# Performance work log

Hardware: AMD Instinct MI355X
Metric: run time of the kernel (lower is better)

The kernel has to match this reference:

```python
import jax, jax.numpy as jnp
import numpy as np

N = 40000   # num_words
H = 384     # hidden_dim
D = 20000   # num_docs
E = 800000  # word-word edges
NNZ = 800000  # doc-word tfidf entries
ALPHA = 0.65
EPS = 1e-5


def layernorm(x, g, b):
    m = jnp.mean(x, axis=-1, keepdims=True)
    v = jnp.mean((x - m) ** 2, axis=-1, keepdims=True)
    return (x - m) * jax.lax.rsqrt(v + EPS) * g + b


def gelu(x):
    return jax.nn.gelu(x, approximate=False)  # torch F.gelu default (erf)


def spmm(rows, cols, vals, M, n_out):
    # COO sparse [n_out, n_in] @ dense [n_in, H]
    return jax.ops.segment_sum(vals[:, None] * M[cols], rows, num_segments=n_out)


def setup_inputs() -> dict:
    key = jax.random.key(0)
    ks = jax.random.split(key, 24)
    s = 1.0 / np.sqrt(H)
    inp = {
        "A_rows": jax.random.randint(ks[0], (E,), 0, N, dtype=jnp.int32),
        "A_cols": jax.random.randint(ks[1], (E,), 0, N, dtype=jnp.int32),
        "A_vals": jax.random.uniform(ks[2], (E,), jnp.float32),
        "X_rows": jax.random.randint(ks[3], (NNZ,), 0, D, dtype=jnp.int32),
        "X_cols": jax.random.randint(ks[4], (NNZ,), 0, N, dtype=jnp.int32),
        "X_vals": jax.random.uniform(ks[5], (NNZ,), jnp.float32),
        "num_docs": D,
        "emb": jax.random.normal(ks[6], (N, H), jnp.float32) * s,
        "W1": jax.random.normal(ks[7], (H, H), jnp.float32) * s,
        "W2": jax.random.normal(ks[8], (H, H), jnp.float32) * s,
        "W3": jax.random.normal(ks[9], (H, H), jnp.float32) * s,
        "g1": jnp.ones((H,), jnp.float32), "b1": jnp.zeros((H,), jnp.float32),
        "g2": jnp.ones((H,), jnp.float32), "b2": jnp.zeros((H,), jnp.float32),
        "g3": jnp.ones((H,), jnp.float32), "b3": jnp.zeros((H,), jnp.float32),
        "mlp_W1": jax.random.normal(ks[10], (H, H), jnp.float32) * s,
        "mlp_b1": jnp.zeros((H,), jnp.float32),
        "mlp_g": jnp.ones((H,), jnp.float32), "mlp_bn": jnp.zeros((H,), jnp.float32),
        "mlp_W2": jax.random.normal(ks[11], (H, H // 2), jnp.float32) * s,
        "mlp_b2": jnp.zeros((H // 2,), jnp.float32),
        "cls_W": jax.random.normal(ks[12], (H // 2, 2), jnp.float32) * s,
        "cls_b": jnp.zeros((2,), jnp.float32),
        "gate_W1": jax.random.normal(ks[13], (2 * H, H), jnp.float32) * s,
        "gate_b1": jnp.zeros((H,), jnp.float32),
        "gate_W2": jax.random.normal(ks[14], (H, H), jnp.float32) * s,
        "gate_b2": jnp.zeros((H,), jnp.float32),
    }
    return inp


def reference(A_rows, A_cols, A_vals, X_rows, X_cols, X_vals, num_docs, emb,
              W1, W2, W3, g1, b1, g2, b2, g3, b3,
              mlp_W1, mlp_b1, mlp_g, mlp_bn, mlp_W2, mlp_b2,
              cls_W, cls_b, gate_W1, gate_b1, gate_W2, gate_b2):
    n = emb.shape[0]
    # --- 3 residual GCN blocks over word graph (eval mode: dropout off) ---
    h = spmm(A_rows, A_cols, A_vals, emb, n)
    h = gelu(layernorm(h @ W1, g1, b1))
    h = spmm(A_rows, A_cols, A_vals, h, n)
    h = gelu(layernorm(h @ W2, g2, b2))
    h = spmm(A_rows, A_cols, A_vals, h, n)
    h = gelu(layernorm(h @ W3, g3, b3))
    word_H = (1.0 - ALPHA) * emb + ALPHA * h
    # --- doc aggregation via TF-IDF SpMM ---
    doc_H = spmm(X_rows, X_cols, X_vals, word_H, num_docs)
    doc_H0 = spmm(X_rows, X_cols, X_vals, emb, num_docs)
    gate_in = jnp.concatenate([doc_H, doc_H0], axis=1)
    gate = jax.nn.sigmoid(gelu(gate_in @ gate_W1 + gate_b1) @ gate_W2 + gate_b2)
    doc = gate * doc_H + (1.0 - gate) * doc_H0
    # --- MLP head ---
    doc = layernorm(gelu(doc @ mlp_W1 + mlp_b1), mlp_g, mlp_bn)
    doc = gelu(doc @ mlp_W2 + mlp_b2)
    logits = doc @ cls_W + cls_b
    return logits
```

## Files before the change

### kernel.cpp

```cpp
#include <hip/hip_runtime.h>
#include <hip/hip_fp16.h>

#define HD 384
#define HHD 192
#define TPR 96
#define RPB 4
#define ECHUNK 128

using bf16x8 = __attribute__((ext_vector_type(8))) short;
using f32x4  = __attribute__((ext_vector_type(4))) float;

__device__ __forceinline__ float gelu_f(float x) {
    return 0.5f * x * (1.0f + erff(x * 0.70710678118654752f));
}

__device__ __forceinline__ float sigmoid_f(float x) {
    return 1.0f / (1.0f + expf(-x));
}

__device__ __forceinline__ void ld_h4(const __half2* p, float2& lo, float2& hi) {
    uint2 raw = *reinterpret_cast<const uint2*>(p);
    lo = __half22float2(*reinterpret_cast<const __half2*>(&raw.x));
    hi = __half22float2(*reinterpret_cast<const __half2*>(&raw.y));
}

__global__ __launch_bounds__(256) void hist_rows(
        const int* __restrict__ rows, int* __restrict__ cnt, int nnz) {
    int e = blockIdx.x * blockDim.x + threadIdx.x;
    if (e < nnz) atomicAdd(&cnt[rows[e]], 1);
}

__global__ __launch_bounds__(256) void scan_local(
        const int* __restrict__ cnt, int* __restrict__ rp,
        int* __restrict__ bsum, int n) {
    __shared__ int wsum[4];
    int i = blockIdx.x * 256 + threadIdx.x;
    int lane = threadIdx.x & 63, wv = threadIdx.x >> 6;
    int v = (i < n) ? cnt[i] : 0;
    int s = v;
    #pragma unroll
    for (int o = 1; o < 64; o <<= 1) {
        int t = __shfl_up(s, o);
        if (lane >= o) s += t;
    }
    if (lane == 63) wsum[wv] = s;
    __syncthreads();
    int woff = 0;
    for (int w = 0; w < wv; ++w) woff += wsum[w];
    if (i < n) rp[i] = woff + s - v;
    if (threadIdx.x == 255) bsum[blockIdx.x] = woff + s;
}

__global__ __launch_bounds__(256) void scan_bsums(
        const int* __restrict__ bsum, int* __restrict__ boff,
        int nb, int* __restrict__ total_out) {
    __shared__ int tmp[256];
    int tid = threadIdx.x;
    int v = (tid < nb) ? bsum[tid] : 0;
    tmp[tid] = v;
    __syncthreads();
    for (int o = 1; o < 256; o <<= 1) {
        int t = (tid >= o) ? tmp[tid - o] : 0;
        __syncthreads();
        tmp[tid] += t;
        __syncthreads();
    }
    if (tid < nb) boff[tid] = tmp[tid] - v;
    if (tid == nb - 1) *total_out = tmp[tid];
}

__global__ __launch_bounds__(256) void scan_add(
        int* __restrict__ rp, const int* __restrict__ boff, int n) {
    int i = blockIdx.x * 256 + threadIdx.x;
    if (i < n) rp[i] += boff[i >> 8];
}

__global__ __launch_bounds__(256) void csr_scatter(
        const int* __restrict__ rows, const int* __restrict__ cols,
        const float* __restrict__ vals, const int* __restrict__ rp,
        int* __restrict__ fill, int* __restrict__ cp,
        float* __restrict__ vp, int nnz) {
    int e = blockIdx.x * blockDim.x + threadIdx.x;
    if (e >= nnz) return;
    int r = rows[e];
    int pos = rp[r] + atomicAdd(&fill[r], 1);
    cp[pos] = cols[e];
    vp[pos] = vals[e];
}

__global__ __launch_bounds__(256) void cvt_fp16(
        const float* __restrict__ in, __half2* __restrict__ out, int n2) {
    int i = blockIdx.x * blockDim.x + threadIdx.x;
    if (i >= n2) return;
    float2 v = reinterpret_cast<const float2*>(in)[i];
    out[i] = __floats2half2_rn(v.x, v.y);
}

__global__ __launch_bounds__(384) void spmm_h2(
        const int* __restrict__ rp, const int* __restrict__ cp,
        const float* __restrict__ vp, const __half2* __restrict__ in,
        __half2* __restrict__ out, int nrows) {
    __shared__ int   lc[RPB][ECHUNK];
    __shared__ float lv[RPB][ECHUNK];
    __shared__ int maxlen_s;
    const int rr = threadIdx.x / TPR;
    const int t  = threadIdx.x % TPR;
    const int r  = blockIdx.x * RPB + rr;
    int s = 0, len = 0;
    if (r < nrows) { s = rp[r]; len = rp[r + 1] - s; }
    if (threadIdx.x == 0) maxlen_s = 0;
    __syncthreads();
    if (t == 0) atomicMax(&maxlen_s, len);
    __syncthreads();
    const int nch = (maxlen_s + ECHUNK - 1) / ECHUNK;
    float a0 = 0.f, a1 = 0.f, a2 = 0.f, a3 = 0.f;
    for (int ch = 0; ch < nch; ++ch) {
        const int base = ch * ECHUNK;
        const int tile = min(ECHUNK, len - base);
        for (int i = t; i < tile; i += TPR) {
            lc[rr][i] = cp[s + base + i];
            lv[rr][i] = vp[s + base + i];
        }
        __syncthreads();
        int p = 0;
        for (; p + 4 <= tile; p += 4) {
            int   c0 = lc[rr][p],     c1 = lc[rr][p + 1];
            int   c2 = lc[rr][p + 2], c3 = lc[rr][p + 3];
            float v0 = lv[rr][p],     v1 = lv[rr][p + 1];
            float v2 = lv[rr][p + 2], v3 = lv[rr][p + 3];
            float2 x0l, x0h, x1l, x1h, x2l, x2h, x3l, x3h;
            ld_h4(in + (size_t)c0 * HHD + 2 * t, x0l, x0h);
            ld_h4(in + (size_t)c1 * HHD + 2 * t, x1l, x1h);
            ld_h4(in + (size_t)c2 * HHD + 2 * t, x2l, x2h);
            ld_h4(in + (size_t)c3 * HHD + 2 * t, x3l, x3h);
            a0 = fmaf(v0, x0l.x, a0); a1 = fmaf(v0, x0l.y, a1);
            a2 = fmaf(v0, x0h.x, a2); a3 = fmaf(v0, x0h.y, a3);
            a0 = fmaf(v1, x1l.x, a0); a1 = fmaf(v1, x1l.y, a1);
            a2 = fmaf(v1, x1h.x, a2); a3 = fmaf(v1, x1h.y, a3);
            a0 = fmaf(v2, x2l.x, a0); a1 = fmaf(v2, x2l.y, a1);
            a2 = fmaf(v2, x2h.x, a2); a3 = fmaf(v2, x2h.y, a3);
            a0 = fmaf(v3, x3l.x, a0); a1 = fmaf(v3, x3l.y, a1);
            a2 = fmaf(v3, x3h.x, a2); a3 = fmaf(v3, x3h.y, a3);
        }
        for (; p < tile; ++p) {
            int c = lc[rr][p];
            float v = lv[rr][p];
            float2 xl, xh;
            ld_h4(in + (size_t)c * HHD + 2 * t, xl, xh);
            a0 = fmaf(v, xl.x, a0); a1 = fmaf(v, xl.y, a1);
            a2 = fmaf(v, xh.x, a2); a3 = fmaf(v, xh.y, a3);
        }
        __syncthreads();
    }
    if (r < nrows) {
        __half2 o0 = __floats2half2_rn(a0, a1);
        __half2 o1 = __floats2half2_rn(a2, a3);
        uint2 packed;
        packed.x = *reinterpret_cast<unsigned*>(&o0);
        packed.y = *reinterpret_cast<unsigned*>(&o1);
        *reinterpret_cast<uint2*>(out + (size_t)r * HHD + 2 * t) = packed;
    }
}

__global__ __launch_bounds__(384) void spmm_doc2(
        const int* __restrict__ rp, const int* __restrict__ cp,
        const float* __restrict__ vp,
        const __half2* __restrict__ inH, const __half2* __restrict__ inE,
        float* __restrict__ docH, float* __restrict__ docH0, int nrows) {
    __shared__ int   lc[RPB][ECHUNK];
    __shared__ float lv[RPB][ECHUNK];
    __shared__ int maxlen_s;
    const int rr = threadIdx.x / TPR;
    const int t  = threadIdx.x % TPR;
    const int r  = blockIdx.x * RPB + rr;
    int s = 0, len = 0;
    if (r < nrows) { s = rp[r]; len = rp[r + 1] - s; }
    if (threadIdx.x == 0) maxlen_s = 0;
    __syncthreads();
    if (t == 0) atomicMax(&maxlen_s, len);
    __syncthreads();
    const int nch = (maxlen_s + ECHUNK - 1) / ECHUNK;
    float h0 = 0.f, h1 = 0.f, h2 = 0.f, h3 = 0.f;
    float e0 = 0.f, e1 = 0.f, e2 = 0.f, e3 = 0.f;
    for (int ch = 0; ch < nch; ++ch) {
        const int base = ch * ECHUNK;
        const int tile = min(ECHUNK, len - base);
        for (int i = t; i < tile; i += TPR) {
            lc[rr][i] = cp[s + base + i];
            lv[rr][i] = vp[s + base + i];
        }
        __syncthreads();
        int p = 0;
        for (; p + 2 <= tile; p += 2) {
            int   c0 = lc[rr][p], c1 = lc[rr][p + 1];
            float v0 = lv[rr][p], v1 = lv[rr][p + 1];
            float2 ha0, hb0, ea0, eb0, ha1, hb1, ea1, eb1;
            ld_h4(inH + (size_t)c0 * HHD + 2 * t, ha0, hb0);
            ld_h4(inE + (size_t)c0 * HHD + 2 * t, ea0, eb0);
            ld_h4(inH + (size_t)c1 * HHD + 2 * t, ha1, hb1);
            ld_h4(inE + (size_t)c1 * HHD + 2 * t, ea1, eb1);
            h0 = fmaf(v0, ha0.x, h0); h1 = fmaf(v0, ha0.y, h1);
            h2 = fmaf(v0, hb0.x, h2); h3 = fmaf(v0, hb0.y, h3);
            e0 = fmaf(v0, ea0.x, e0); e1 = fmaf(v0, ea0.y, e1);
            e2 = fmaf(v0, eb0.x, e2); e3 = fmaf(v0, eb0.y, e3);
            h0 = fmaf(v1, ha1.x, h0); h1 = fmaf(v1, ha1.y, h1);
            h2 = fmaf(v1, hb1.x, h2); h3 = fmaf(v1, hb1.y, h3);
            e0 = fmaf(v1, ea1.x, e0); e1 = fmaf(v1, ea1.y, e1);
            e2 = fmaf(v1, eb1.x, e2); e3 = fmaf(v1, eb1.y, e3);
        }
        for (; p < tile; ++p) {
            int c = lc[rr][p];
            float v = lv[rr][p];
            float2 ha, hb, ea, eb;
            ld_h4(inH + (size_t)c * HHD + 2 * t, ha, hb);
            ld_h4(inE + (size_t)c * HHD + 2 * t, ea, eb);
            h0 = fmaf(v, ha.x, h0); h1 = fmaf(v, ha.y, h1);
            h2 = fmaf(v, hb.x, h2); h3 = fmaf(v, hb.y, h3);
            e0 = fmaf(v, ea.x, e0); e1 = fmaf(v, ea.y, e1);
            e2 = fmaf(v, eb.x, e2); e3 = fmaf(v, eb.y, e3);
        }
        __syncthreads();
    }
    if (r < nrows) {
        float4 ev = make_float4(e0, e1, e2, e3);
        float4 hv = make_float4(0.35f * e0 + 0.65f * h0, 0.35f * e1 + 0.65f * h1,
                                0.35f * e2 + 0.65f * h2, 0.35f * e3 + 0.65f * h3);
        *reinterpret_cast<float4*>(docH0 + (size_t)r * HD + 4 * t) = ev;
        *reinterpret_cast<float4*>(docH  + (size_t)r * HD + 4 * t) = hv;
    }
}

__global__ __launch_bounds__(256) void pack_w(
        const float* __restrict__ W, unsigned short* __restrict__ out,
        int KS, int NS, int N) {
    int t = blockIdx.x * 256 + threadIdx.x;
    int total = KS * NS * 64;
    if (t >= total) return;
    int l = t & 63;
    int ns = (t >> 6) % NS;
    int ks = t / (64 * NS);
    int col = ns * 16 + (l & 15);
    int k0 = ks * 32 + 8 * (l >> 4);
    size_t obase = (size_t)t * 8;
    size_t pstride = (size_t)KS * NS * 512;
    #pragma unroll
    for (int e = 0; e < 8; ++e) {
        float f = W[(size_t)(k0 + e) * N + col];
        unsigned u = __float_as_uint(f);
        unsigned short h = (unsigned short)(u >> 16);
        float r = f - __uint_as_float(u & 0xFFFF0000u);
        unsigned short lo = (unsigned short)(__float_as_uint(r) >> 16);
        out[obase + e] = (unsigned short)h;
        out[pstride + obase + e] = lo;
    }
}

__device__ __forceinline__ void splitf(const float* f, bf16x8& h, bf16x8& l) {
    #pragma unroll
    for (int e = 0; e < 8; ++e) {
        unsigned u = __float_as_uint(f[e]);
        h[e] = (short)(unsigned short)(u >> 16);
        float r = f[e] - __uint_as_float(u & 0xFFFF0000u);
        l[e] = (short)(unsigned short)(__float_as_uint(r) >> 16);
    }
}

template<int MODE, int NS, int KS, int KSPLIT, bool A16, bool OUT16>
__global__ __launch_bounds__(256) void gemm_mfma(
        const float* __restrict__ A1, const float* __restrict__ A2,
        const unsigned short* __restrict__ Wp,
        const float* __restrict__ bias, const float* __restrict__ gamma,
        const float* __restrict__ beta,
        const float* __restrict__ aux1, const float* __restrict__ aux2,
        float* __restrict__ out, int M) {
    constexpr int N = NS * 16;
    constexpr int NSW = NS / 4;
    const int tid = threadIdx.x;
    const int wave = tid >> 6, l = tid & 63;
    const int row_base = blockIdx.x * 16;
    const int arow = row_base + (l & 15);
    const bool arow_ok = arow < M;
    const int koff = 8 * (l >> 4);
    const size_t pstride = (size_t)KS * NS * 512;

    __shared__ float ps[4][16], pq[4][16];
    __shared__ float mean_s[16], rstd_s[16];
    __shared__ float plg[4][16][2];

    f32x4 acc[NSW];
    #pragma unroll
    for (int ns = 0; ns < NSW; ++ns)
        acc[ns] = f32x4{0.f, 0.f, 0.f, 0.f};

    for (int ks = 0; ks < KS; ++ks) {
        const float* Ap;
        int ksl;
        if (ks < KSPLIT) { Ap = A1; ksl = ks; }
        else             { Ap = A2; ksl = ks - KSPLIT; }
        bf16x8 ah, al;
        if (arow_ok) {
            float f[8];
            if constexpr (A16) {
                const __half2* src = reinterpret_cast<const __half2*>(Ap)
                                     + ((size_t)arow * HD + ksl * 32 + koff) / 2;
                #pragma unroll
                for (int e = 0; e < 4; ++e) {
                    float2 v = __half22float2(src[e]);
                    f[2 * e]     = v.x;
                    f[2 * e + 1] = v.y;
                }
            } else {
                const float* src = Ap + (size_t)arow * HD + ksl * 32 + koff;
                float4 a0 = *reinterpret_cast<const float4*>(src);
                float4 a1 = *reinterpret_cast<const float4*>(src + 4);
                f[0] = a0.x; f[1] = a0.y; f[2] = a0.z; f[3] = a0.w;
                f[4] = a1.x; f[5] = a1.y; f[6] = a1.z; f[7] = a1.w;
            }
            splitf(f, ah, al);
        } else {
            #pragma unroll
            for (int e = 0; e < 8; ++e) { ah[e] = 0; al[e] = 0; }
        }
        const unsigned short* Bp = Wp + (size_t)ks * NS * 512
                                   + (size_t)wave * NSW * 512 + (size_t)l * 8;
        #pragma unroll
        for (int ns = 0; ns < NSW; ++ns) {
            bf16x8 bh = *reinterpret_cast<const bf16x8*>(Bp + ns * 512);
            bf16x8 bl = *reinterpret_cast<const bf16x8*>(Bp + pstride + ns * 512);
            acc[ns] = __builtin_amdgcn_mfma_f32_16x16x32_bf16(ah, bh, acc[ns], 0, 0, 0);
            acc[ns] = __builtin_amdgcn_mfma_f32_16x16x32_bf16(al, bh, acc[ns], 0, 0, 0);
            acc[ns] = __builtin_amdgcn_mfma_f32_16x16x32_bf16(ah, bl, acc[ns], 0, 0, 0);
        }
    }

    const int col_lane = l & 15;
    const int g4 = (l >> 4) * 4;
    constexpr float invN = 1.0f / (float)N;

    if constexpr (MODE == 0 || MODE == 3) {
        if constexpr (MODE == 3) {
            #pragma unroll
            for (int ns = 0; ns < NSW; ++ns) {
                float bb = bias[(wave * NSW + ns) * 16 + col_lane];
                #pragma unroll
                for (int r = 0; r < 4; ++r)
                    acc[ns][r] = gelu_f(acc[ns][r] + bb);
            }
        }
        float s[4] = {0.f, 0.f, 0.f, 0.f}, q[4] = {0.f, 0.f, 0.f, 0.f};
        #pragma unroll
        for (int ns = 0; ns < NSW; ++ns)
            #pragma unroll
            for (int r = 0; r < 4; ++r) {
                float v = acc[ns][r];
                s[r] += v;
                q[r] += v * v;
            }
        #pragma unroll
        for (int r = 0; r < 4; ++r) {
            #pragma unroll
            for (int m = 1; m < 16; m <<= 1) {
                s[r] += __shfl_xor(s[r], m);
                q[r] += __shfl_xor(q[r], m);
            }
        }
        if (col_lane == 0) {
            #pragma unroll
            for (int r = 0; r < 4; ++r) {
                ps[wave][g4 + r] = s[r];
                pq[wave][g4 + r] = q[r];
            }
        }
        __syncthreads();
        if (tid < 16) {
            float ss = ps[0][tid] + ps[1][tid] + ps[2][tid] + ps[3][tid];
            float qq = pq[0][tid] + pq[1][tid] + pq[2][tid] + pq[3][tid];
            float m = ss * invN;
            mean_s[tid] = m;
            rstd_s[tid] = rsqrtf(qq * invN - m * m + 1e-5f);
        }
        __syncthreads();
        #pragma unroll
        for (int ns = 0; ns < NSW; ++ns) {
            int col = (wave * NSW + ns) * 16 + col_lane;
            float gg = gamma[col], bb = beta[col];
            #pragma unroll
            for (int r = 0; r < 4; ++r) {
                int row = row_base + g4 + r;
                if (row < M) {
                    float y = (acc[ns][r] - mean_s[g4 + r]) * rstd_s[g4 + r] * gg + bb;
                    if constexpr (MODE == 0) {
                        y = gelu_f(y);
                        if constexpr (OUT16)
                            reinterpret_cast<__half*>(out)[(size_t)row * N + col] =
                                __float2half(y);
                        else
                            out[(size_t)row * N + col] = y;
                    } else {
                        out[(size_t)row * N + col] = y;
                    }
                }
            }
        }
    } else if constexpr (MODE == 1) {
        #pragma unroll
        for (int ns = 0; ns < NSW; ++ns) {
            int col = (wave * NSW + ns) * 16 + col_lane;
            float bb = bias[col];
            #pragma unroll
            for (int r = 0; r < 4; ++r) {
                int row = row_base + g4 + r;
                if (row < M)
                    out[(size_t)row * N + col] = gelu_f(acc[ns][r] + bb);
            }
        }
    } else if constexpr (MODE == 2) {
        #pragma unroll
        for (int ns = 0; ns < NSW; ++ns) {
            int col = (wave * NSW + ns) * 16 + col_lane;
            float bb = bias[col];
            #pragma unroll
            for (int r = 0; r < 4; ++r) {
                int row = row_base + g4 + r;
                if (row < M) {
                    float g = sigmoid_f(acc[ns][r] + bb);
                    float h1 = aux1[(size_t)row * N + col];
                    float h0 = aux2[(size_t)row * N + col];
                    out[(size_t)row * N + col] = g * h1 + (1.0f - g) * h0;
                }
            }
        }
    } else if constexpr (MODE == 4) {
        float lg0[4] = {0.f, 0.f, 0.f, 0.f}, lg1[4] = {0.f, 0.f, 0.f, 0.f};
        #pragma unroll
        for (int ns = 0; ns < NSW; ++ns) {
            int col = (wave * NSW + ns) * 16 + col_lane;
            float bb = bias[col];
            float c0 = aux1[col * 2 + 0];
            float c1 = aux1[col * 2 + 1];
            #pragma unroll
            for (int r = 0; r < 4; ++r) {
                float v = gelu_f(acc[ns][r] + bb);
                lg0[r] = fmaf(v, c0, lg0[r]);
                lg1[r] = fmaf(v, c1, lg1[r]);
            }
        }
        #pragma unroll
        for (int r = 0; r < 4; ++r) {
            #pragma unroll
            for (int m = 1; m < 16; m <<= 1) {
                lg0[r] += __shfl_xor(lg0[r], m);
                lg1[r] += __shfl_xor(lg1[r], m);
            }
        }
        if (col_lane == 0) {
            #pragma unroll
            for (int r = 0; r < 4; ++r) {
                plg[wave][g4 + r][0] = lg0[r];
                plg[wave][g4 + r][1] = lg1[r];
            }
        }
        __syncthreads();
        if (tid < 32) {
            int rloc = tid >> 1, c = tid & 1;
            int row = row_base + rloc;
            if (row < M) {
                float t = plg[0][rloc][c] + plg[1][rloc][c]
                        + plg[2][rloc][c] + plg[3][rloc][c];
                out[(size_t)row * 2 + c] = t + gamma[c];
            }
        }
    }
}

static void build_csr(const int* rows, const int* cols, const float* vals,
                      int nnz, int n, int* rp, int* cp, float* vp,
                      int* cnt, int* bsum, int* boff, hipStream_t stream) {
    hipMemsetAsync(cnt, 0, (size_t)n * sizeof(int), stream);
    hist_rows<<<(nnz + 255) / 256, 256, 0, stream>>>(rows, cnt, nnz);
    int nb = (n + 255) / 256;
    scan_local<<<nb, 256, 0, stream>>>(cnt, rp, bsum, n);
    scan_bsums<<<1, 256, 0, stream>>>(bsum, boff, nb, rp + n);
    scan_add<<<nb, 256, 0, stream>>>(rp, boff, n);
    hipMemsetAsync(cnt, 0, (size_t)n * sizeof(int), stream);
    csr_scatter<<<(nnz + 255) / 256, 256, 0, stream>>>(rows, cols, vals, rp, cnt, cp, vp, nnz);
}

extern "C" void kernel_launch(void* const* d_in, const int* in_sizes, int n_in,
                              void* d_out, int out_size, void* d_ws, size_t ws_size,
                              hipStream_t stream) {
    const int*   A_rows = (const int*)  d_in[0];
    const int*   A_cols = (const int*)  d_in[1];
    const float* A_vals = (const float*)d_in[2];
    const int*   X_rows = (const int*)  d_in[3];
    const int*   X_cols = (const int*)  d_in[4];
    const float* X_vals = (const float*)d_in[5];
    const float* emb    = (const float*)d_in[7];
    const float* W1     = (const float*)d_in[8];
    const float* W2     = (const float*)d_in[9];
    const float* W3     = (const float*)d_in[10];
    const float* g1     = (const float*)d_in[11];
    const float* b1     = (const float*)d_in[12];
    const float* g2     = (const float*)d_in[13];
    const float* b2     = (const float*)d_in[14];
    const float* g3     = (const float*)d_in[15];
    const float* b3     = (const float*)d_in[16];
    const float* mW1    = (const float*)d_in[17];
    const float* mb1    = (const float*)d_in[18];
    const float* mg     = (const float*)d_in[19];
    const float* mbn    = (const float*)d_in[20];
    const float* mW2    = (const float*)d_in[21];
    const float* mb2    = (const float*)d_in[22];
    const float* cW     = (const float*)d_in[23];
    const float* cb     = (const float*)d_in[24];
    const float* gW1    = (const float*)d_in[25];
    const float* gb1    = (const float*)d_in[26];
    const float* gW2    = (const float*)d_in[27];
    const float* gb2    = (const float*)d_in[28];

    const int E_   = in_sizes[0];
    const int NNZ_ = in_sizes[3];
    const int N_   = in_sizes[7] / HD;
    const int D_   = out_size / 2;

    __half2* emb16 = (__half2*)d_ws;
    __half2* Ba    = emb16 + (size_t)N_ * HHD;
    __half2* Bb    = Ba    + (size_t)N_ * HHD;
    float* docH0 = (float*)(Bb + (size_t)N_ * HHD);
    int*   A_rp = (int*)(docH0 + (size_t)D_ * HD);
    int*   A_cp = A_rp + (N_ + 1);
    float* A_vp = (float*)(A_cp + E_);
    int*   X_rp = (int*)(A_vp + E_);
    int*   X_cp = X_rp + (D_ + 1);
    float* X_vp = (float*)(X_cp + NNZ_);
    int*   cnt  = (int*)(X_vp + NNZ_);
    int*   bsum = cnt + N_;
    int*   boff = bsum + 256;
    size_t pk_off = ((size_t)(boff + 256 - (int*)d_ws) + 7) & ~(size_t)7;
    unsigned short* packs = (unsigned short*)((float*)d_ws + pk_off);
    const size_t SZ_SQ = (size_t)2 * HD * HD;
    unsigned short* p_W1  = packs;
    unsigned short* p_W2  = p_W1  + SZ_SQ;
    unsigned short* p_W3  = p_W2  + SZ_SQ;
    unsigned short* p_gW2 = p_W3  + SZ_SQ;
    unsigned short* p_mW1 = p_gW2 + SZ_SQ;
    unsigned short* p_gW1 = p_mW1 + SZ_SQ;
    unsigned short* p_mW2 = p_gW1 + (size_t)2 * 2 * HD * HD;

    float* docH  = (float*)Ba;
    float* t1    = (float*)emb16;
    float* dmix  = (float*)Bb;
    float* un    = (float*)Ba;
    float* logits = (float*)d_out;

    const int word_grid = (N_ + 15) / 16;
    const int doc_grid  = (D_ + 15) / 16;
    const int spmm_word_grid = (N_ + RPB - 1) / RPB;
    const int spmm_doc_grid  = (D_ + RPB - 1) / RPB;

    pack_w<<<(12 * 24 * 64 + 255) / 256, 256, 0, stream>>>(W1,  p_W1,  12, 24, HD);
    pack_w<<<(12 * 24 * 64 + 255) / 256, 256, 0, stream>>>(W2,  p_W2,  12, 24, HD);
    pack_w<<<(12 * 24 * 64 + 255) / 256, 256, 0, stream>>>(W3,  p_W3,  12, 24, HD);
    pack_w<<<(12 * 24 * 64 + 255) / 256, 256, 0, stream>>>(gW2, p_gW2, 12, 24, HD);
    pack_w<<<(12 * 24 * 64 + 255) / 256, 256, 0, stream>>>(mW1, p_mW1, 12, 24, HD);
    pack_w<<<(24 * 24 * 64 + 255) / 256, 256, 0, stream>>>(gW1, p_gW1, 24, 24, HD);
    pack_w<<<(12 * 12 * 64 + 255) / 256, 256, 0, stream>>>(mW2, p_mW2, 12, 12, HHD);

    cvt_fp16<<<((N_ * HHD) + 255) / 256, 256, 0, stream>>>(emb, emb16, N_ * HHD);

    build_csr(A_rows, A_cols, A_vals, E_, N_, A_rp, A_cp, A_vp, cnt, bsum, boff, stream);
    build_csr(X_rows, X_cols, X_vals, NNZ_, D_, X_rp, X_cp, X_vp, cnt, bsum, boff, stream);

    spmm_h2<<<spmm_word_grid, 384, 0, stream>>>(A_rp, A_cp, A_vp, emb16, Ba, N_);
    gemm_mfma<0, 24, 12, 12, true, true><<<word_grid, 256, 0, stream>>>(
        (const float*)Ba, nullptr, p_W1, nullptr, g1, b1, nullptr, nullptr, (float*)Bb, N_);
    spmm_h2<<<spmm_word_grid, 384, 0, stream>>>(A_rp, A_cp, A_vp, Bb, Ba, N_);
    gemm_mfma<0, 24, 12, 12, true, true><<<word_grid, 256, 0, stream>>>(
        (const float*)Ba, nullptr, p_W2, nullptr, g2, b2, nullptr, nullptr, (float*)Bb, N_);
    spmm_h2<<<spmm_word_grid, 384, 0, stream>>>(A_rp, A_cp, A_vp, Bb, Ba, N_);
    gemm_mfma<0, 24, 12, 12, true, true><<<word_grid, 256, 0, stream>>>(
        (const float*)Ba, nullptr, p_W3, nullptr, g3, b3, nullptr, nullptr, (float*)Bb, N_);

    spmm_doc2<<<spmm_doc_grid, 384, 0, stream>>>(X_rp, X_cp, X_vp, Bb, emb16,
                                                 docH, docH0, D_);

    gemm_mfma<1, 24, 24, 12, false, false><<<doc_grid, 256, 0, stream>>>(
        docH, docH0, p_gW1, gb1, nullptr, nullptr, nullptr, nullptr, t1, D_);
    gemm_mfma<2, 24, 12, 12, false, false><<<doc_grid, 256, 0, stream>>>(
        t1, nullptr, p_gW2, gb2, nullptr, nullptr, docH, docH0, dmix, D_);
    gemm_mfma<3, 24, 12, 12, false, false><<<doc_grid, 256, 0, stream>>>(
        dmix, nullptr, p_mW1, mb1, mg, mbn, nullptr, nullptr, un, D_);
    gemm_mfma<4, 12, 12, 12, false, false><<<doc_grid, 256, 0, stream>>>(
        un, nullptr, p_mW2, mb2, cb, nullptr, cW, nullptr, logits, D_);
}
```

Measured before the change: 1.129 ms.

## Interleave word_H and emb in one fp16 buffer and widen SpMM loads

```diff
diff --git a/kernel.cpp b/kernel.cpp
--- a/kernel.cpp
+++ b/kernel.cpp
@@ -3,9 +3,11 @@
 
 #define HD 384
 #define HHD 192
-#define TPR 96
-#define RPB 4
 #define ECHUNK 128
+#define WTPR 48
+#define WRPB 8
+#define DTPR 96
+#define DRPB 4
 
 using bf16x8 = __attribute__((ext_vector_type(8))) short;
 using f32x4  = __attribute__((ext_vector_type(4))) float;
@@ -18,10 +20,14 @@
     return 1.0f / (1.0f + expf(-x));
 }
 
-__device__ __forceinline__ void ld_h4(const __half2* p, float2& lo, float2& hi) {
-    uint2 raw = *reinterpret_cast<const uint2*>(p);
-    lo = __half22float2(*reinterpret_cast<const __half2*>(&raw.x));
-    hi = __half22float2(*reinterpret_cast<const __half2*>(&raw.y));
+__device__ __forceinline__ void fma8(float* a, uint4 q, float v) {
+    const __half2* h = reinterpret_cast<const __half2*>(&q);
+    #pragma unroll
+    for (int k = 0; k < 4; ++k) {
+        float2 f = __half22float2(h[k]);
+        a[2 * k]     = fmaf(v, f.x, a[2 * k]);
+        a[2 * k + 1] = fmaf(v, f.y, a[2 * k + 1]);
+    }
 }
 
 __global__ __launch_bounds__(256) void hist_rows(
@@ -88,24 +94,25 @@
     vp[pos] = vals[e];
 }
 
-__global__ __launch_bounds__(256) void cvt_fp16(
-        const float* __restrict__ in, __half2* __restrict__ out, int n2) {
+__global__ __launch_bounds__(256) void cvt_fp16s(
+        const float* __restrict__ in, __half2* __restrict__ cmb, int n2) {
     int i = blockIdx.x * blockDim.x + threadIdx.x;
     if (i >= n2) return;
+    int row = i / HHD, col = i % HHD;
     float2 v = reinterpret_cast<const float2*>(in)[i];
-    out[i] = __floats2half2_rn(v.x, v.y);
+    cmb[(size_t)row * (2 * HHD) + HHD + col] = __floats2half2_rn(v.x, v.y);
 }
 
 __global__ __launch_bounds__(384) void spmm_h2(
         const int* __restrict__ rp, const int* __restrict__ cp,
-        const float* __restrict__ vp, const __half2* __restrict__ in,
-        __half2* __restrict__ out, int nrows) {
-    __shared__ int   lc[RPB][ECHUNK];
-    __shared__ float lv[RPB][ECHUNK];
+        const float* __restrict__ vp, const __half* __restrict__ in,
+        long instride, long inoff, __half* __restrict__ out, int nrows) {
+    __shared__ int   lc[WRPB][ECHUNK];
+    __shared__ float lv[WRPB][ECHUNK];
     __shared__ int maxlen_s;
-    const int rr = threadIdx.x / TPR;
-    const int t  = threadIdx.x % TPR;
-    const int r  = blockIdx.x * RPB + rr;
+    const int rr = threadIdx.x / WTPR;
+    const int t  = threadIdx.x % WTPR;
+    const int r  = blockIdx.x * WRPB + rr;
     int s = 0, len = 0;
     if (r < nrows) { s = rp[r]; len = rp[r + 1] - s; }
     if (threadIdx.x == 0) maxlen_s = 0;
@@ -113,66 +120,57 @@
     if (t == 0) atomicMax(&maxlen_s, len);
     __syncthreads();
     const int nch = (maxlen_s + ECHUNK - 1) / ECHUNK;
-    float a0 = 0.f, a1 = 0.f, a2 = 0.f, a3 = 0.f;
+    float a[8] = {0.f, 0.f, 0.f, 0.f, 0.f, 0.f, 0.f, 0.f};
+    const long lane_off = inoff + t * 8;
     for (int ch = 0; ch < nch; ++ch) {
         const int base = ch * ECHUNK;
         const int tile = min(ECHUNK, len - base);
-        for (int i = t; i < tile; i += TPR) {
+        for (int i = t; i < tile; i += WTPR) {
             lc[rr][i] = cp[s + base + i];
             lv[rr][i] = vp[s + base + i];
         }
         __syncthreads();
         int p = 0;
         for (; p + 4 <= tile; p += 4) {
-            int   c0 = lc[rr][p],     c1 = lc[rr][p + 1];
-            int   c2 = lc[rr][p + 2], c3 = lc[rr][p + 3];
-            float v0 = lv[rr][p],     v1 = lv[rr][p + 1];
-            float v2 = lv[rr][p + 2], v3 = lv[rr][p + 3];
-            float2 x0l, x0h, x1l, x1h, x2l, x2h, x3l, x3h;
-            ld_h4(in + (size_t)c0 * HHD + 2 * t, x0l, x0h);
-            ld_h4(in + (size_t)c1 * HHD + 2 * t, x1l, x1h);
-            ld_h4(in + (size_t)c2 * HHD + 2 * t, x2l, x2h);
-            ld_h4(in + (size_t)c3 * HHD + 2 * t, x3l, x3h);
-            a0 = fmaf(v0, x0l.x, a0); a1 = fmaf(v0, x0l.y, a1);
-            a2 = fmaf(v0, x0h.x, a2); a3 = fmaf(v0, x0h.y, a3);
-            a0 = fmaf(v1, x1l.x, a0); a1 = fmaf(v1, x1l.y, a1);
-            a2 = fmaf(v1, x1h.x, a2); a3 = fmaf(v1, x1h.y, a3);
-            a0 = fmaf(v2, x2l.x, a0); a1 = fmaf(v2, x2l.y, a1);
-            a2 = fmaf(v2, x2h.x, a2); a3 = fmaf(v2, x2h.y, a3);
-            a0 = fmaf(v3, x3l.x, a0); a1 = fmaf(v3, x3l.y, a1);
-            a2 = fmaf(v3, x3h.x, a2); a3 = fmaf(v3, x3h.y, a3);
+            uint4 q0 = *reinterpret_cast<const uint4*>(in + (size_t)lc[rr][p]     * instride + lane_off);
+            uint4 q1 = *reinterpret_cast<const uint4*>(in + (size_t)lc[rr][p + 1] * instride + lane_off);
+            uint4 q2 = *reinterpret_cast<const uint4*>(in + (size_t)lc[rr][p + 2] * instride + lane_off);
+            uint4 q3 = *reinterpret_cast<const uint4*>(in + (size_t)lc[rr][p + 3] * instride + lane_off);
+            fma8(a, q0, lv[rr][p]);
+            fma8(a, q1, lv[rr][p + 1]);
+            fma8(a, q2, lv[rr][p + 2]);
+            fma8(a, q3, lv[rr][p + 3]);
         }
         for (; p < tile; ++p) {
-            int c = lc[rr][p];
-            float v = lv[rr][p];
-            float2 xl, xh;
-            ld_h4(in + (size_t)c * HHD + 2 * t, xl, xh);
-            a0 = fmaf(v, xl.x, a0); a1 = fmaf(v, xl.y, a1);
-            a2 = fmaf(v, xh.x, a2); a3 = fmaf(v, xh.y, a3);
+            uint4 q = *reinterpret_cast<const uint4*>(in + (size_t)lc[rr][p] * instride + lane_off);
+            fma8(a, q, lv[rr][p]);
         }
         __syncthreads();
     }
     if (r < nrows) {
-        __half2 o0 = __floats2half2_rn(a0, a1);
-        __half2 o1 = __floats2half2_rn(a2, a3);
-        uint2 packed;
-        packed.x = *reinterpret_cast<unsigned*>(&o0);
-        packed.y = *reinterpret_cast<unsigned*>(&o1);
-        *reinterpret_cast<uint2*>(out + (size_t)r * HHD + 2 * t) = packed;
+        __half2 o0 = __floats2half2_rn(a[0], a[1]);
+        __half2 o1 = __floats2half2_rn(a[2], a[3]);
+        __half2 o2 = __floats2half2_rn(a[4], a[5]);
+        __half2 o3 = __floats2half2_rn(a[6], a[7]);
+        uint4 pk;
+        pk.x = *reinterpret_cast<unsigned*>(&o0);
+        pk.y = *reinterpret_cast<unsigned*>(&o1);
+        pk.z = *reinterpret_cast<unsigned*>(&o2);
+        pk.w = *reinterpret_cast<unsigned*>(&o3);
+        *reinterpret_cast<uint4*>(out + (size_t)r * HD + t * 8) = pk;
     }
 }
 
 __global__ __launch_bounds__(384) void spmm_doc2(
         const int* __restrict__ rp, const int* __restrict__ cp,
-        const float* __restrict__ vp,
-        const __half2* __restrict__ inH, const __half2* __restrict__ inE,
+        const float* __restrict__ vp, const __half* __restrict__ cmb,
         float* __restrict__ docH, float* __restrict__ docH0, int nrows) {
-    __shared__ int   lc[RPB][ECHUNK];
-    __shared__ float lv[RPB][ECHUNK];
+    __shared__ int   lc[DRPB][ECHUNK];
+    __shared__ float lv[DRPB][ECHUNK];
     __shared__ int maxlen_s;
-    const int rr = threadIdx.x / TPR;
-    const int t  = threadIdx.x % TPR;
-    const int r  = blockIdx.x * RPB + rr;
+    const int rr = threadIdx.x / DTPR;
+    const int t  = threadIdx.x % DTPR;
+    const int r  = blockIdx.x * DRPB + rr;
     int s = 0, len = 0;
     if (r < nrows) { s = rp[r]; len = rp[r + 1] - s; }
     if (threadIdx.x == 0) maxlen_s = 0;
@@ -180,53 +178,38 @@
     if (t == 0) atomicMax(&maxlen_s, len);
     __syncthreads();
     const int nch = (maxlen_s + ECHUNK - 1) / ECHUNK;
-    float h0 = 0.f, h1 = 0.f, h2 = 0.f, h3 = 0.f;
-    float e0 = 0.f, e1 = 0.f, e2 = 0.f, e3 = 0.f;
+    float a[8] = {0.f, 0.f, 0.f, 0.f, 0.f, 0.f, 0.f, 0.f};
+    const long lane_off = t * 8;
     for (int ch = 0; ch < nch; ++ch) {
         const int base = ch * ECHUNK;
         const int tile = min(ECHUNK, len - base);
-        for (int i = t; i < tile; i += TPR) {
+        for (int i = t; i < tile; i += DTPR) {
             lc[rr][i] = cp[s + base + i];
             lv[rr][i] = vp[s + base + i];
         }
         __syncthreads();
         int p = 0;
-        for (; p + 2 <= tile; p += 2) {
-            int   c0 = lc[rr][p], c1 = lc[rr][p + 1];
-            float v0 = lv[rr][p], v1 = lv[rr][p + 1];
-            float2 ha0, hb0, ea0, eb0, ha1, hb1, ea1, eb1;
-            ld_h4(inH + (size_t)c0 * HHD + 2 * t, ha0, hb0);
-            ld_h4(inE + (size_t)c0 * HHD + 2 * t, ea0, eb0);
-            ld_h4(inH + (size_t)c1 * HHD + 2 * t, ha1, hb1);
-            ld_h4(inE + (size_t)c1 * HHD + 2 * t, ea1, eb1);
-            h0 = fmaf(v0, ha0.x, h0); h1 = fmaf(v0, ha0.y, h1);
-            h2 = fmaf(v0, hb0.x, h2); h3 = fmaf(v0, hb0.y, h3);
-            e0 = fmaf(v0, ea0.x, e0); e1 = fmaf(v0, ea0.y, e1);
-            e2 = fmaf(v0, eb0.x, e2); e3 = fmaf(v0, eb0.y, e3);
-            h0 = fmaf(v1, ha1.x, h0); h1 = fmaf(v1, ha1.y, h1);
-            h2 = fmaf(v1, hb1.x, h2); h3 = fmaf(v1, hb1.y, h3);
-            e0 = fmaf(v1, ea1.x, e0); e1 = fmaf(v1, ea1.y, e1);
-            e2 = fmaf(v1, eb1.x, e2); e3 = fmaf(v1, eb1.y, e3);
+        for (; p + 4 <= tile; p += 4) {
+            uint4 q0 = *reinterpret_cast<const uint4*>(cmb + (size_t)lc[rr][p]     * (2 * HD) + lane_off);
+            uint4 q1 = *reinterpret_cast<const uint4*>(cmb + (size_t)lc[rr][p + 1] * (2 * HD) + lane_off);
+            uint4 q2 = *reinterpret_cast<const uint4*>(cmb + (size_t)lc[rr][p + 2] * (2 * HD) + lane_off);
+            uint4 q3 = *reinterpret_cast<const uint4*>(cmb + (size_t)lc[rr][p + 3] * (2 * HD) + lane_off);
+            fma8(a, q0, lv[rr][p]);
+            fma8(a, q1, lv[rr][p + 1]);
+            fma8(a, q2, lv[rr][p + 2]);
+            fma8(a, q3, lv[rr][p + 3]);
         }
         for (; p < tile; ++p) {
-            int c = lc[rr][p];
-            float v = lv[rr][p];
-            float2 ha, hb, ea, eb;
-            ld_h4(inH + (size_t)c * HHD + 2 * t, ha, hb);
-            ld_h4(inE + (size_t)c * HHD + 2 * t, ea, eb);
-            h0 = fmaf(v, ha.x, h0); h1 = fmaf(v, ha.y, h1);
-            h2 = fmaf(v, hb.x, h2); h3 = fmaf(v, hb.y, h3);
-            e0 = fmaf(v, ea.x, e0); e1 = fmaf(v, ea.y, e1);
-            e2 = fmaf(v, eb.x, e2); e3 = fmaf(v, eb.y, e3);
+            uint4 q = *reinterpret_cast<const uint4*>(cmb + (size_t)lc[rr][p] * (2 * HD) + lane_off);
+            fma8(a, q, lv[rr][p]);
         }
         __syncthreads();
     }
     if (r < nrows) {
-        float4 ev = make_float4(e0, e1, e2, e3);
-        float4 hv = make_float4(0.35f * e0 + 0.65f * h0, 0.35f * e1 + 0.65f * h1,
-                                0.35f * e2 + 0.65f * h2, 0.35f * e3 + 0.65f * h3);
-        *reinterpret_cast<float4*>(docH0 + (size_t)r * HD + 4 * t) = ev;
-        *reinterpret_cast<float4*>(docH  + (size_t)r * HD + 4 * t) = hv;
+        float* dst = (t < 48) ? docH  + (size_t)r * HD + t * 8
+                              : docH0 + (size_t)r * HD + (t - 48) * 8;
+        *reinterpret_cast<float4*>(dst)     = make_float4(a[0], a[1], a[2], a[3]);
+        *reinterpret_cast<float4*>(dst + 4) = make_float4(a[4], a[5], a[6], a[7]);
     }
 }
 
@@ -337,7 +320,7 @@
     const int g4 = (l >> 4) * 4;
     constexpr float invN = 1.0f / (float)N;
 
-    if constexpr (MODE == 0 || MODE == 3) {
+    if constexpr (MODE == 0 || MODE == 3 || MODE == 5) {
         if constexpr (MODE == 3) {
             #pragma unroll
             for (int ns = 0; ns < NSW; ++ns) {
@@ -396,6 +379,12 @@
                                 __float2half(y);
                         else
                             out[(size_t)row * N + col] = y;
+                    } else if constexpr (MODE == 5) {
+                        float yy = gelu_f(y);
+                        const __half* ch = reinterpret_cast<const __half*>(aux1);
+                        float ev = __half2float(ch[(size_t)row * (2 * HD) + HD + col]);
+                        reinterpret_cast<__half*>(out)[(size_t)row * (2 * HD) + col] =
+                            __float2half(0.35f * ev + 0.65f * yy);
                     } else {
                         out[(size_t)row * N + col] = y;
                     }
@@ -523,11 +512,10 @@
     const int N_   = in_sizes[7] / HD;
     const int D_   = out_size / 2;
 
-    __half2* emb16 = (__half2*)d_ws;
-    __half2* Ba    = emb16 + (size_t)N_ * HHD;
-    __half2* Bb    = Ba    + (size_t)N_ * HHD;
-    float* docH0 = (float*)(Bb + (size_t)N_ * HHD);
-    int*   A_rp = (int*)(docH0 + (size_t)D_ * HD);
+    __half* cmb = (__half*)d_ws;
+    __half* Ba  = cmb + (size_t)N_ * 2 * HD;
+    __half* Bb  = Ba  + (size_t)N_ * HD;
+    int*   A_rp = (int*)(Bb + (size_t)N_ * HD);
     int*   A_cp = A_rp + (N_ + 1);
     float* A_vp = (float*)(A_cp + E_);
     int*   X_rp = (int*)(A_vp + E_);
@@ -548,15 +536,16 @@
     unsigned short* p_mW2 = p_gW1 + (size_t)2 * 2 * HD * HD;
 
     float* docH  = (float*)Ba;
-    float* t1    = (float*)emb16;
-    float* dmix  = (float*)Bb;
+    float* docH0 = (float*)Bb;
+    float* t1    = (float*)cmb;
+    float* dmix  = (float*)cmb + (size_t)D_ * HD;
     float* un    = (float*)Ba;
     float* logits = (float*)d_out;
 
     const int word_grid = (N_ + 15) / 16;
     const int doc_grid  = (D_ + 15) / 16;
-    const int spmm_word_grid = (N_ + RPB - 1) / RPB;
-    const int spmm_doc_grid  = (D_ + RPB - 1) / RPB;
+    const int spmm_word_grid = (N_ + WRPB - 1) / WRPB;
+    const int spmm_doc_grid  = (D_ + DRPB - 1) / DRPB;
 
     pack_w<<<(12 * 24 * 64 + 255) / 256, 256, 0, stream>>>(W1,  p_W1,  12, 24, HD);
     pack_w<<<(12 * 24 * 64 + 255) / 256, 256, 0, stream>>>(W2,  p_W2,  12, 24, HD);
@@ -566,23 +555,23 @@
     pack_w<<<(24 * 24 * 64 + 255) / 256, 256, 0, stream>>>(gW1, p_gW1, 24, 24, HD);
     pack_w<<<(12 * 12 * 64 + 255) / 256, 256, 0, stream>>>(mW2, p_mW2, 12, 12, HHD);
 
-    cvt_fp16<<<((N_ * HHD) + 255) / 256, 256, 0, stream>>>(emb, emb16, N_ * HHD);
+    cvt_fp16s<<<((N_ * HHD) + 255) / 256, 256, 0, stream>>>(emb, (__half2*)cmb, N_ * HHD);
 
     build_csr(A_rows, A_cols, A_vals, E_, N_, A_rp, A_cp, A_vp, cnt, bsum, boff, stream);
     build_csr(X_rows, X_cols, X_vals, NNZ_, D_, X_rp, X_cp, X_vp, cnt, bsum, boff, stream);
 
-    spmm_h2<<<spmm_word_grid, 384, 0, stream>>>(A_rp, A_cp, A_vp, emb16, Ba, N_);
+    spmm_h2<<<spmm_word_grid, 384, 0, stream>>>(A_rp, A_cp, A_vp, cmb, 2 * HD, HD, Ba, N_);
     gemm_mfma<0, 24, 12, 12, true, true><<<word_grid, 256, 0, stream>>>(
         (const float*)Ba, nullptr, p_W1, nullptr, g1, b1, nullptr, nullptr, (float*)Bb, N_);
-    spmm_h2<<<spmm_word_grid, 384, 0, stream>>>(A_rp, A_cp, A_vp, Bb, Ba, N_);
+    spmm_h2<<<spmm_word_grid, 384, 0, stream>>>(A_rp, A_cp, A_vp, Bb, HD, 0, Ba, N_);
     gemm_mfma<0, 24, 12, 12, true, true><<<word_grid, 256, 0, stream>>>(
         (const float*)Ba, nullptr, p_W2, nullptr, g2, b2, nullptr, nullptr, (float*)Bb, N_);
-    spmm_h2<<<spmm_word_grid, 384, 0, stream>>>(A_rp, A_cp, A_vp, Bb, Ba, N_);
-    gemm_mfma<0, 24, 12, 12, true, true><<<word_grid, 256, 0, stream>>>(
-        (const float*)Ba, nullptr, p_W3, nullptr, g3, b3, nullptr, nullptr, (float*)Bb, N_);
-
-    spmm_doc2<<<spmm_doc_grid, 384, 0, stream>>>(X_rp, X_cp, X_vp, Bb, emb16,
-                                                 docH, docH0, D_);
+    spmm_h2<<<spmm_word_grid, 384, 0, stream>>>(A_rp, A_cp, A_vp, Bb, HD, 0, Ba, N_);
+    gemm_mfma<5, 24, 12, 12, true, true><<<word_grid, 256, 0, stream>>>(
+        (const float*)Ba, nullptr, p_W3, nullptr, g3, b3, (const float*)cmb, nullptr,
+        (float*)cmb, N_);
+
+    spmm_doc2<<<spmm_doc_grid, 384, 0, stream>>>(X_rp, X_cp, X_vp, cmb, docH, docH0, D_);
 
     gemm_mfma<1, 24, 24, 12, false, false><<<doc_grid, 256, 0, stream>>>(
         docH, docH0, p_gW1, gb1, nullptr, nullptr, nullptr, nullptr, t1, D_);
```

Result: no change. 1.150 ms (+1.8%).
